# Optimization experiments

Measured on AMD Instinct MI355X. Metric: run time of the kernel, lower is better.

Reference implementation:

```python
import jax, jax.numpy as jnp
import numpy as np

DIM = 512; D_STATE = 8; D_CONV = 3; EXPAND = 1; WIN = 7; N = WIN * WIN
D_INNER = EXPAND * DIM; D_HALF = D_INNER // 2
DT_RANK = -(-DIM // 16)  # 32
E = DT_RANK + 2 * D_STATE  # 48
B_WIN = 512


def _diag_flat(w):
    idx = []
    for s in range(2 * w - 1):
        for r in range(max(0, s - (w - 1)), min(w - 1, s) + 1):
            idx.append(r * w + (s - r))
    return np.array(idx, dtype=np.int32)


def _anti_flat(w):
    idx = []
    for s in range(2 * w - 1):
        for r in range(max(0, s - (w - 1)), min(w - 1, s) + 1):
            c = s - r
            idx.append(r * w + (w - 1 - c))
    return np.array(idx, dtype=np.int32)

DIAG_IDX = jnp.asarray(_diag_flat(WIN))
ANTI_IDX = jnp.asarray(_anti_flat(WIN))
V_IDX = jnp.asarray(np.arange(N).reshape(WIN, WIN).T.reshape(-1).astype(np.int32))


def setup_inputs() -> dict:
    key = jax.random.key(0)
    ks = iter(jax.random.split(key, 32))
    f32 = jnp.float32
    def lin_w(k, out_d, in_d):
        return (jax.random.normal(k, (out_d, in_d), f32) * (in_d ** -0.5)).astype(f32)
    inp = {}
    inp['tokens'] = jax.random.normal(next(ks), (B_WIN, N, DIM), f32)
    for nm in ['pre_h', 'pre_v', 'pre_d', 'pre_a', 'post_h', 'post_v', 'post_d', 'post_a']:
        inp[nm + '_w'] = lin_w(next(ks), DIM, DIM)
        inp[nm + '_b'] = jnp.zeros((DIM,), f32)
    inp['in_proj_w'] = lin_w(next(ks), D_INNER, DIM)
    inp['conv_x_w'] = jax.random.normal(next(ks), (D_HALF, 1, D_CONV), f32) * (D_CONV ** -0.5)
    inp['conv_x_b'] = jnp.zeros((D_HALF,), f32)
    inp['conv_z_w'] = jax.random.normal(next(ks), (D_HALF, 1, D_CONV), f32) * (D_CONV ** -0.5)
    inp['conv_z_b'] = jnp.zeros((D_HALF,), f32)
    inp['x_proj_w'] = lin_w(next(ks), E, D_HALF)
    inp['ln_w'] = jnp.ones((E,), f32)
    inp['ln_b'] = jnp.zeros((E,), f32)
    dt_std = DT_RANK ** -0.5
    inp['dt_proj_w'] = jax.random.uniform(next(ks), (D_HALF, DT_RANK), f32, -dt_std, dt_std)
    u = jax.random.uniform(next(ks), (D_HALF,), f32)
    dt = jnp.clip(jnp.exp(u * (np.log(0.1) - np.log(0.001)) + np.log(0.001)), 1e-4, None)
    inp['dt_proj_b'] = dt + jnp.log(-jnp.expm1(-dt))
    inp['A_log'] = jnp.tile(jnp.log(jnp.arange(1, D_STATE + 1, dtype=f32))[None, :], (D_HALF, 1))
    inp['D_param'] = jnp.ones((D_HALF,), f32)
    inp['out_proj_w'] = lin_w(next(ks), DIM, D_INNER)
    inp['gate_logits'] = jnp.zeros((4,), f32)
    return inp


def _linear(x, W, b=None):
    y = x @ W.T
    return y if b is None else y + b


def _dwconv_same(x, w, b):
    # x: (b, d, l), w: (d, 1, k) depthwise, cross-correlation like torch
    y = jax.lax.conv_general_dilated(x, w, window_strides=(1,), padding='SAME',
                                     dimension_numbers=('NCH', 'OIH', 'NCH'),
                                     feature_group_count=x.shape[1])
    return y + b[None, :, None]


def _layernorm(x, g, b, eps=1e-5):
    m = jnp.mean(x, -1, keepdims=True)
    v = jnp.var(x, -1, keepdims=True)
    return (x - m) * jax.lax.rsqrt(v + eps) * g + b


def _selective_scan(u, delta, A, Bm, Cm, D, delta_bias):
    # u, delta: (b,d,l); A: (d,n); Bm, Cm: (b,n,l); D: (d,)
    delta = jax.nn.softplus(delta + delta_bias[None, :, None])
    u_l = jnp.moveaxis(u, 2, 0)       # (l,b,d)
    d_l = jnp.moveaxis(delta, 2, 0)   # (l,b,d)
    B_l = jnp.moveaxis(Bm, 2, 0)      # (l,b,n)
    C_l = jnp.moveaxis(Cm, 2, 0)      # (l,b,n)
    h0 = jnp.zeros((u.shape[0], u.shape[1], A.shape[1]), u.dtype)  # (b,d,n)

    def step(h, t):
        dt_t, u_t, B_t, C_t = t
        dA = jnp.exp(dt_t[:, :, None] * A[None])          # (b,d,n)
        dBu = dt_t[:, :, None] * B_t[:, None, :] * u_t[:, :, None]
        h = h * dA + dBu
        y = jnp.einsum('bdn,bn->bd', h, C_t)
        return h, y

    _, ys = jax.lax.scan(step, h0, (d_l, u_l, B_l, C_l))
    y = jnp.moveaxis(ys, 0, 2)  # (b,d,l)
    return y + D[None, :, None] * u


def _mamba_core(x_seq, p):
    b, L, _ = x_seq.shape
    xz = _linear(x_seq, p['in_proj_w'])              # (b,l,d_inner)
    xz = jnp.swapaxes(xz, 1, 2)                      # (b,d_inner,l)
    x, z = jnp.split(xz, 2, axis=1)                  # each (b,d_half,l)
    x_conv = jax.nn.silu(_dwconv_same(x, p['conv_x_w'], p['conv_x_b']))
    z_conv = jax.nn.silu(_dwconv_same(z, p['conv_z_w'], p['conv_z_b']))
    A = -jnp.exp(p['A_log'])
    x_dbl = jnp.einsum('bdl,ed->ble', x_conv, p['x_proj_w'])  # (b,l,E)
    x_dbl = _layernorm(x_dbl, p['ln_w'], p['ln_b'])
    dt, Bm, Cm = jnp.split(x_dbl, [DT_RANK, DT_RANK + D_STATE], axis=-1)
    dt = jnp.swapaxes(_linear(dt, p['dt_proj_w']), 1, 2)      # (b,d_half,l)
    Bm = jnp.swapaxes(Bm, 1, 2)                                # (b,n,l)
    Cm = jnp.swapaxes(Cm, 1, 2)
    y = _selective_scan(x_conv, dt, A, Bm, Cm, p['D_param'], p['dt_proj_b'])
    y = jnp.nan_to_num(y)
    y = jnp.concatenate([y, z_conv], axis=1)                   # (b,d_inner,l)
    y = jnp.swapaxes(y, 1, 2)
    return _linear(y, p['out_proj_w'])


def reference(tokens, pre_h_w, pre_h_b, pre_v_w, pre_v_b, pre_d_w, pre_d_b,
              pre_a_w, pre_a_b, in_proj_w, conv_x_w, conv_x_b, conv_z_w, conv_z_b,
              x_proj_w, ln_w, ln_b, dt_proj_w, dt_proj_b, A_log, D_param,
              out_proj_w, post_h_w, post_h_b, post_v_w, post_v_b, post_d_w,
              post_d_b, post_a_w, post_a_b, gate_logits):
    p = dict(in_proj_w=in_proj_w, conv_x_w=conv_x_w, conv_x_b=conv_x_b,
             conv_z_w=conv_z_w, conv_z_b=conv_z_b, x_proj_w=x_proj_w,
             ln_w=ln_w, ln_b=ln_b, dt_proj_w=dt_proj_w, dt_proj_b=dt_proj_b,
             A_log=A_log, D_param=D_param, out_proj_w=out_proj_w)
    rh = _linear(tokens, pre_h_w, pre_h_b)
    rv = _linear(tokens, pre_v_w, pre_v_b)[:, V_IDX, :]
    rd = _linear(tokens, pre_d_w, pre_d_b)[:, DIAG_IDX, :]
    ra = _linear(tokens, pre_a_w, pre_a_b)[:, ANTI_IDX, :]
    r_all = jnp.concatenate([rh, rv, rd, ra], axis=0)
    y_all = _mamba_core(r_all, p)
    yh, yv, yd, ya = jnp.split(y_all, 4, axis=0)
    yh = _linear(yh, post_h_w, post_h_b)
    yv = _linear(yv, post_v_w, post_v_b)
    yd = _linear(yd, post_d_w, post_d_b)
    ya = _linear(ya, post_a_w, post_a_b)
    g = jax.nn.softmax(gate_logits)
    return g[0] * yh + g[1] * yv + g[2] * yd + g[3] * ya
```

## Files before the change

kernel.cpp:

```cpp
#include <hip/hip_runtime.h>
#include <stdint.h>

typedef __attribute__((ext_vector_type(8))) short bf16x8;
typedef __attribute__((ext_vector_type(4))) float f32x4;

__device__ __forceinline__ float bf2f(short u){
  union { float f; uint32_t i; } v; v.i = ((uint32_t)(uint16_t)u) << 16; return v.f;
}
__device__ __forceinline__ short f2bf(float x){
  union { float f; uint32_t i; } v; v.f = x;
  uint32_t r = v.i + 0x7FFFu + ((v.i >> 16) & 1u);
  return (short)(r >> 16);
}

__device__ __forceinline__ void gl_lds16(const short* g, short* l){
  __builtin_amdgcn_global_load_lds(
      (__attribute__((address_space(1))) void*)(short*)g,
      (__attribute__((address_space(3))) void*)l, 16, 0, 0);
}

__device__ const int d_DIAG[49] = {0,1,7,2,8,14,3,9,15,21,4,10,16,22,28,5,11,17,23,29,35,
  6,12,18,24,30,36,42,13,19,25,31,37,43,20,26,32,38,44,27,33,39,45,34,40,46,41,47,48};
__device__ const int d_ANTI[49] = {6,5,13,4,12,20,3,11,19,27,2,10,18,26,34,1,9,17,25,33,41,
  0,8,16,24,32,40,48,7,15,23,31,39,47,14,22,30,38,46,21,29,37,45,28,36,44,35,43,42};

__device__ __forceinline__ int perm_idx(int g, int l){
  if (g == 0) return l;
  if (g == 1) return (l % 7) * 7 + l / 7;
  if (g == 2) return d_DIAG[l];
  return d_ANTI[l];
}

template<int NT>
__device__ __forceinline__ void kloop_pf(
    const short* a0, const short* a1, const short* b0, const short* b1,
    int lds0, int lds1, short* As, short* Bs,
    int quad, int mr, int wm, int wn, f32x4 acc[4][4])
{
  auto STAGE = [&](int t){
    int b = t % 3;
    gl_lds16(a0 + t*32, As + b*4096 + lds0);
    gl_lds16(a1 + t*32, As + b*4096 + lds1);
    gl_lds16(b0 + t*32, Bs + b*4096 + lds0);
    gl_lds16(b1 + t*32, Bs + b*4096 + lds1);
  };
  int sw = (quad ^ ((mr >> 1) & 3)) * 8;
  STAGE(0); STAGE(1);
  for (int t = 0; t < NT; ++t){
    if (t + 2 < NT){
      STAGE(t + 2);
      asm volatile("s_waitcnt vmcnt(8)" ::: "memory");
    } else if (t + 1 < NT){
      asm volatile("s_waitcnt vmcnt(4)" ::: "memory");
    } else {
      asm volatile("s_waitcnt vmcnt(0)" ::: "memory");
    }
    __builtin_amdgcn_s_barrier();
    __builtin_amdgcn_sched_barrier(0);
    const short* Ab = As + (t % 3) * 4096;
    const short* Bb = Bs + (t % 3) * 4096;
    bf16x8 af[4], bfr[4];
    #pragma unroll
    for (int x = 0; x < 4; x++){
      af[x]  = *(const bf16x8*)(Ab + (wm + x*16 + mr)*32 + sw);
      bfr[x] = *(const bf16x8*)(Bb + (wn + x*16 + mr)*32 + sw);
    }
    #pragma unroll
    for (int mt = 0; mt < 4; mt++)
      #pragma unroll
      for (int nt2 = 0; nt2 < 4; nt2++)
        acc[mt][nt2] = __builtin_amdgcn_mfma_f32_16x16x32_bf16(af[mt], bfr[nt2], acc[mt][nt2],0,0,0);
    __builtin_amdgcn_sched_barrier(0);
    __builtin_amdgcn_s_barrier();
  }
}

__global__ __launch_bounds__(256) void k_conv_all(
    const float* __restrict__ in_proj,
    const float* __restrict__ pw0, const float* __restrict__ pw1,
    const float* __restrict__ pw2, const float* __restrict__ pw3,
    const float* __restrict__ xpw, const float* __restrict__ dtw,
    short* __restrict__ inp_bf, short* __restrict__ postw_bf,
    short* __restrict__ xpw_bf, short* __restrict__ dtw_bf)
{
  int q = blockIdx.x*256 + threadIdx.x;
  const float* src; short* dst; int off;
  if (q < 65536){ src = in_proj; dst = inp_bf; off = q; }
  else if (q < 65536 + 262144){
    int r = q - 65536; int g = r >> 16; int loc = r & 65535;
    src = (g==0)?pw0:(g==1)?pw1:(g==2)?pw2:pw3;
    dst = postw_bf + g*262144; off = loc;
  }
  else if (q < 65536 + 262144 + 3072){ src = xpw; dst = xpw_bf; off = q - (65536+262144); }
  else { src = dtw; dst = dtw_bf; off = q - (65536+262144+3072); }
  float4 v = *(const float4*)(src + off*4);
  uint32_t p0 = (uint32_t)(uint16_t)f2bf(v.x) | ((uint32_t)(uint16_t)f2bf(v.y) << 16);
  uint32_t p1 = (uint32_t)(uint16_t)f2bf(v.z) | ((uint32_t)(uint16_t)f2bf(v.w) << 16);
  uint2 p; p.x = p0; p.y = p1;
  *(uint2*)(dst + off*4) = p;
}

__global__ __launch_bounds__(256) void k_transp(
    const float* __restrict__ pw0, const float* __restrict__ pw1,
    const float* __restrict__ pw2, const float* __restrict__ pw3,
    const float* __restrict__ outp,
    short* __restrict__ wpreT, short* __restrict__ woutT)
{
  __shared__ float tile[64][65];
  int which = blockIdx.y;
  const float* src = (which==0)?pw0:(which==1)?pw1:(which==2)?pw2:(which==3)?pw3:outp;
  short* dst = (which < 4) ? (wpreT + which*262144) : woutT;
  int bi = blockIdx.x >> 3, bj = blockIdx.x & 7;
  int r0 = bi*64, c0 = bj*64;
  int t = threadIdx.x;
  int row = t >> 2, cg = t & 3;
  const float4* s4 = (const float4*)(src + (r0+row)*512 + c0 + cg*16);
  #pragma unroll
  for (int i=0;i<4;i++){
    float4 v = s4[i];
    tile[row][cg*16 + i*4 + 0] = v.x;
    tile[row][cg*16 + i*4 + 1] = v.y;
    tile[row][cg*16 + i*4 + 2] = v.z;
    tile[row][cg*16 + i*4 + 3] = v.w;
  }
  __syncthreads();
  int oc = t >> 2;
  short tmp[16];
  #pragma unroll
  for (int i=0;i<16;i++) tmp[i] = f2bf(tile[cg*16 + i][oc]);
  short* dp = dst + (size_t)(c0+oc)*512 + r0 + cg*16;
  *(bf16x8*)(dp)     = *(bf16x8*)tmp;
  *(bf16x8*)(dp + 8) = *((bf16x8*)tmp + 1);
}

__global__ __launch_bounds__(256) void k_tok(const float* __restrict__ t, short* __restrict__ o){
  int i = (blockIdx.x*256 + threadIdx.x) * 4;
  float4 v = *(const float4*)(t + i);
  uint32_t p0 = (uint32_t)(uint16_t)f2bf(v.x) | ((uint32_t)(uint16_t)f2bf(v.y) << 16);
  uint32_t p1 = (uint32_t)(uint16_t)f2bf(v.z) | ((uint32_t)(uint16_t)f2bf(v.w) << 16);
  uint2 p; p.x = p0; p.y = p1;
  *(uint2*)(o + i) = p;
}

__global__ __launch_bounds__(256) void k_bxz_gains(const float* __restrict__ in_proj,
    const float* __restrict__ b0, const float* __restrict__ b1,
    const float* __restrict__ b2, const float* __restrict__ b3,
    const float* __restrict__ gl,
    const float* __restrict__ pb0, const float* __restrict__ pb1,
    const float* __restrict__ pb2, const float* __restrict__ pb3,
    float* __restrict__ bxz, float* __restrict__ gains, float* __restrict__ biasc)
{
  if (blockIdx.x < 8){
    int idx = blockIdx.x*256 + threadIdx.x;
    int g = idx >> 9, i = idx & 511;
    const float* bb = (g==0)?b0:(g==1)?b1:(g==2)?b2:b3;
    float s = 0.f;
    for (int t=0;t<512;t++) s += in_proj[i*512+t]*bb[t];
    bxz[idx] = s;
  } else {
    float m = fmaxf(fmaxf(gl[0], gl[1]), fmaxf(gl[2], gl[3]));
    float e0 = expf(gl[0]-m), e1 = expf(gl[1]-m), e2 = expf(gl[2]-m), e3 = expf(gl[3]-m);
    float s = e0+e1+e2+e3;
    float g0 = e0/s, g1 = e1/s, g2 = e2/s, g3 = e3/s;
    int t = threadIdx.x;
    if (t == 0){ gains[0]=g0; gains[1]=g1; gains[2]=g2; gains[3]=g3; }
    biasc[t]     = g0*pb0[t]     + g1*pb1[t]     + g2*pb2[t]     + g3*pb3[t];
    biasc[t+256] = g0*pb0[t+256] + g1*pb1[t+256] + g2*pb2[t+256] + g3*pb3[t+256];
  }
}

__device__ __forceinline__ void mfma_2x4_k(const short* a0, const short* a1,
    const short* b0, const short* b1, const short* b2, const short* b3,
    int K, f32x4 acc[2][4])
{
  for (int k0 = 0; k0 < K; k0 += 32){
    bf16x8 av0 = *(const bf16x8*)(a0 + k0);
    bf16x8 av1 = *(const bf16x8*)(a1 + k0);
    bf16x8 bv0 = *(const bf16x8*)(b0 + k0);
    bf16x8 bv1 = *(const bf16x8*)(b1 + k0);
    bf16x8 bv2 = *(const bf16x8*)(b2 + k0);
    bf16x8 bv3 = *(const bf16x8*)(b3 + k0);
    acc[0][0] = __builtin_amdgcn_mfma_f32_16x16x32_bf16(av0, bv0, acc[0][0],0,0,0);
    acc[0][1] = __builtin_amdgcn_mfma_f32_16x16x32_bf16(av0, bv1, acc[0][1],0,0,0);
    acc[0][2] = __builtin_amdgcn_mfma_f32_16x16x32_bf16(av0, bv2, acc[0][2],0,0,0);
    acc[0][3] = __builtin_amdgcn_mfma_f32_16x16x32_bf16(av0, bv3, acc[0][3],0,0,0);
    acc[1][0] = __builtin_amdgcn_mfma_f32_16x16x32_bf16(av1, bv0, acc[1][0],0,0,0);
    acc[1][1] = __builtin_amdgcn_mfma_f32_16x16x32_bf16(av1, bv1, acc[1][1],0,0,0);
    acc[1][2] = __builtin_amdgcn_mfma_f32_16x16x32_bf16(av1, bv2, acc[1][2],0,0,0);
    acc[1][3] = __builtin_amdgcn_mfma_f32_16x16x32_bf16(av1, bv3, acc[1][3],0,0,0);
  }
}

__global__ __launch_bounds__(256) void k_wfuse(const short* __restrict__ inp_bf,
    const short* __restrict__ wpreT, const short* __restrict__ postw_bf,
    const short* __restrict__ woutT, const float* __restrict__ gains,
    short* __restrict__ wxz, short* __restrict__ wogc)
{
  int z = blockIdx.z; int g = z & 3, which = z >> 2;
  int bn = blockIdx.x * 64, bm = blockIdx.y * 128;
  int lane = threadIdx.x & 63, wave = threadIdx.x >> 6;
  int mr = lane & 15, qk = (lane >> 4) * 8, quad = lane >> 4;
  const short* Am = which ? (postw_bf + g*262144) : inp_bf;
  const short* Bm = which ? woutT : (wpreT + g*262144);
  const short* a0 = Am + (bm + wave*32 + mr)*512 + qk;
  const short* a1 = a0 + 16*512;
  const short* b0 = Bm + (bn +  0 + mr)*512 + qk;
  const short* b1 = Bm + (bn + 16 + mr)*512 + qk;
  const short* b2 = Bm + (bn + 32 + mr)*512 + qk;
  const short* b3 = Bm + (bn + 48 + mr)*512 + qk;
  f32x4 acc[2][4] = {};
  mfma_2x4_k(a0, a1, b0, b1, b2, b3, 512, acc);
  float gain = which ? gains[g] : 1.f;
  #pragma unroll
  for (int s=0;s<2;s++)
    #pragma unroll
    for (int t=0;t<4;t++)
      #pragma unroll
      for (int r=0;r<4;r++){
        int row = bm + wave*32 + s*16 + quad*4 + r;
        int col = bn + t*16 + mr;
        if (which) wogc[row*2048 + g*512 + col] = f2bf(gain * acc[s][t][r]);
        else       wxz[g*262144 + row*512 + col] = f2bf(acc[s][t][r]);
      }
}

__global__ __launch_bounds__(256) void k_gemm1(const short* __restrict__ tok,
    const short* __restrict__ wxz, const float* __restrict__ bxz, short* __restrict__ xz)
{
  __shared__ __align__(16) short As[12288];
  __shared__ __align__(16) short Bs[12288];
  int g = blockIdx.z;
  int bid = blockIdx.x;
  int swz = (bid & 7) * 98 + (bid >> 3);
  int bn = (swz & 3) * 128, bm = (swz >> 2) * 128;
  int tid = threadIdx.x, lane = tid & 63, wave = tid >> 6;

  const short* aG[2]; const short* bG[2]; int ldsOff[2];
  #pragma unroll
  for (int i = 0; i < 2; i++){
    int c = wave*2 + i;
    int r = c*16 + (lane >> 2);
    int ch = ((lane & 3) ^ ((lane >> 3) & 3)) * 8;
    int grow = bm + r;
    int b = grow / 49, l = grow - b*49;
    int sl = perm_idx(g, l);
    aG[i] = tok + ((size_t)(b*49 + sl))*512 + ch;
    bG[i] = wxz + (size_t)g*262144 + (size_t)(bn + r)*512 + ch;
    ldsOff[i] = c*512;
  }

  int mr = lane & 15, quad = lane >> 4;
  int wm = (wave & 1)*64, wn = (wave >> 1)*64;
  f32x4 acc[4][4] = {};

  kloop_pf<16>(aG[0], aG[1], bG[0], bG[1], ldsOff[0], ldsOff[1],
               As, Bs, quad, mr, wm, wn, acc);

  #pragma unroll
  for (int mt = 0; mt < 4; mt++)
    #pragma unroll
    for (int rr = 0; rr < 4; rr++){
      int row = bm + wm + mt*16 + quad*4 + rr;
      int b = row / 49, l = row - b*49;
      size_t orow = ((size_t)(g*512 + b)*49 + l)*512;
      #pragma unroll
      for (int nt = 0; nt < 4; nt++){
        int col = bn + wn + nt*16 + mr;
        xz[orow + col] = f2bf(acc[mt][nt][rr] + bxz[g*512 + col]);
      }
    }
}

__global__ __launch_bounds__(256) void k_conv(const short* __restrict__ xz,
    const float* __restrict__ cxw, const float* __restrict__ cxb,
    const float* __restrict__ czw, const float* __restrict__ czb,
    short* __restrict__ ycat)
{
  int t = threadIdx.x;
  int oct = t & 63, lstart = t >> 6;
  int ch0 = oct * 8;
  bool isx = ch0 < 256;
  int cc0 = isx ? ch0 : ch0 - 256;
  const float* wsrc = isx ? cxw : czw;
  const float* bsrc = isx ? cxb : czb;
  float w0[8], w1[8], w2[8], bb[8];
  #pragma unroll
  for (int e=0;e<8;e++){
    w0[e] = wsrc[(cc0+e)*3]; w1[e] = wsrc[(cc0+e)*3+1]; w2[e] = wsrc[(cc0+e)*3+2];
    bb[e] = bsrc[cc0+e];
  }
  int gb = blockIdx.x; int g = gb >> 9, b = gb & 511;
  const short* src = xz + (size_t)gb*25088 + ch0;
  short* dst = ycat + (size_t)(b*49)*2048 + g*512 + ch0;
  for (int l = lstart; l < 49; l += 4){
    bf16x8 vm = {}, vp = {};
    bf16x8 v0 = *(const bf16x8*)(src + l*512);
    if (l > 0)  vm = *(const bf16x8*)(src + (l-1)*512);
    if (l < 48) vp = *(const bf16x8*)(src + (l+1)*512);
    short ov[8];
    #pragma unroll
    for (int e=0;e<8;e++){
      float x = w0[e]*bf2f(vm[e]) + w1[e]*bf2f(v0[e]) + w2[e]*bf2f(vp[e]) + bb[e];
      ov[e] = f2bf(x / (1.f + __expf(-x)));
    }
    *(bf16x8*)(dst + l*2048) = *(bf16x8*)ov;
  }
}

__global__ __launch_bounds__(256) void k_xproj(const short* __restrict__ ycat,
    const short* __restrict__ xpw_bf, const float* __restrict__ lnw, const float* __restrict__ lnb,
    const short* __restrict__ dtw_bf, const float* __restrict__ dtb,
    short* __restrict__ dtln, float* __restrict__ bc)
{
  __shared__ __align__(16) char smem[36864];
  float* xd = (float*)smem;
  short* xln = (short*)(smem + 26624);

  int bm = blockIdx.x * 128;
  int g = bm / 25088;
  int tid = threadIdx.x, lane = tid & 63, w = tid >> 6;
  int mr = lane & 15, quad = lane >> 4, qk = quad * 8;

  {
    const short* ap[2];
    #pragma unroll
    for (int s=0;s<2;s++)
      ap[s] = ycat + (size_t)(bm - g*25088 + w*32 + s*16 + mr)*2048 + g*512 + qk;
    f32x4 acc[2][3] = {};
    #pragma unroll
    for (int k0 = 0; k0 < 256; k0 += 32){
      bf16x8 av[2];
      #pragma unroll
      for (int s=0;s<2;s++) av[s] = *(const bf16x8*)(ap[s] + k0);
      #pragma unroll
      for (int t=0;t<3;t++){
        bf16x8 bv = *(const bf16x8*)(xpw_bf + (t*16 + mr)*256 + qk + k0);
        #pragma unroll
        for (int s=0;s<2;s++)
          acc[s][t] = __builtin_amdgcn_mfma_f32_16x16x32_bf16(av[s], bv, acc[s][t],0,0,0);
      }
    }
    #pragma unroll
    for (int s=0;s<2;s++)
      #pragma unroll
      for (int t=0;t<3;t++)
        #pragma unroll
        for (int r=0;r<4;r++)
          xd[(w*32 + s*16 + quad*4 + r)*52 + t*16 + mr] = acc[s][t][r];
  }
  __syncthreads();

  if (tid < 128){
    f32x4* xr4 = (f32x4*)(xd + tid*52);
    f32x4 s = xr4[0];
    #pragma unroll
    for (int i=1;i<12;i++) s += xr4[i];
    float m = (s[0]+s[1]+s[2]+s[3]) * (1.f/48.f);
    f32x4 vs = {};
    #pragma unroll
    for (int i=0;i<12;i++){ f32x4 d = xr4[i] - m; vs += d*d; }
    float var = (vs[0]+vs[1]+vs[2]+vs[3]) * (1.f/48.f);
    float rstd = rsqrtf(var + 1e-5f);
    const f32x4* g4 = (const f32x4*)lnw;
    const f32x4* b4 = (const f32x4*)lnb;
    uint32_t* xlr = (uint32_t*)(xln + tid*40);
    #pragma unroll
    for (int i=0;i<8;i++){
      f32x4 v = (xr4[i] - m) * rstd * g4[i] + b4[i];
      xlr[2*i]   = (uint32_t)(uint16_t)f2bf(v[0]) | ((uint32_t)(uint16_t)f2bf(v[1]) << 16);
      xlr[2*i+1] = (uint32_t)(uint16_t)f2bf(v[2]) | ((uint32_t)(uint16_t)f2bf(v[3]) << 16);
    }
    f32x4* bco = (f32x4*)(bc + (size_t)(bm + tid)*16);
    #pragma unroll
    for (int i=8;i<12;i++)
      bco[i-8] = (xr4[i] - m) * rstd * g4[i] + b4[i];
  }
  __syncthreads();

  {
    bf16x8 a[2];
    #pragma unroll
    for (int s=0;s<2;s++)
      a[s] = *(const bf16x8*)(xln + (w*32 + s*16 + mr)*40 + qk);
    #pragma unroll 4
    for (int nt=0; nt<16; nt++){
      int col = nt*16 + mr;
      bf16x8 bv = *(const bf16x8*)(dtw_bf + col*32 + qk);
      float dtbv = dtb[col];
      #pragma unroll
      for (int s=0;s<2;s++){
        f32x4 acc = {};
        acc = __builtin_amdgcn_mfma_f32_16x16x32_bf16(a[s], bv, acc,0,0,0);
        #pragma unroll
        for (int r=0;r<4;r++){
          int grow = bm + w*32 + s*16 + quad*4 + r;
          float dtv = acc[r] + dtbv;
          float e  = __expf(dtv);
          float sp = __logf(1.f + e);
          float delta = (dtv > 15.f) ? dtv : sp;
          dtln[(size_t)grow*256 + col] = f2bf(delta);
        }
      }
    }
  }
}

__global__ __launch_bounds__(256) void k_scan(short* __restrict__ ycat,
    const short* __restrict__ dtln, const float* __restrict__ bc,
    const float* __restrict__ Alog, const float* __restrict__ Dp)
{
  __shared__ __align__(16) float bcs[784];
  int gb = blockIdx.x; int g = gb >> 9, b = gb & 511;
  int d = threadIdx.x;
  if (d < 196) ((f32x4*)bcs)[d] = ((const f32x4*)(bc + (size_t)gb*784))[d];
  __syncthreads();

  float A[8], h[8];
  {
    f32x4 a0 = *(const f32x4*)(Alog + d*8);
    f32x4 a1 = *(const f32x4*)(Alog + d*8 + 4);
    #pragma unroll
    for (int n=0;n<4;n++){ A[n] = -__expf(a0[n]); A[n+4] = -__expf(a1[n]); h[n]=0.f; h[n+4]=0.f; }
  }
  float Dpar = Dp[d];

  const short* dptr = dtln + (size_t)gb*49*256 + d;
  short* uptr = ycat + (size_t)(b*49)*2048 + g*512 + d;

  float dn = bf2f(dptr[0]);
  float un = bf2f(uptr[0]);
  for (int l=0;l<49;l++){
    float delta = dn, u = un;
    if (l < 48){ dn = bf2f(dptr[(l+1)*256]); un = bf2f(uptr[(l+1)*2048]); }
    const f32x4* bcr = (const f32x4*)(bcs + l*16);
    f32x4 B0 = bcr[0], B1 = bcr[1], C0 = bcr[2], C1 = bcr[3];
    float du = delta * u;
    float y = 0.f;
    #pragma unroll
    for (int n=0;n<4;n++){
      h[n] = h[n]*__expf(delta*A[n]) + du*B0[n];
      y += h[n]*C0[n];
    }
    #pragma unroll
    for (int n=0;n<4;n++){
      h[n+4] = h[n+4]*__expf(delta*A[n+4]) + du*B1[n];
      y += h[n+4]*C1[n];
    }
    uptr[l*2048] = f2bf(y + Dpar*u);
  }
}

__global__ __launch_bounds__(256) void k_gemmF(const short* __restrict__ ycat,
    const short* __restrict__ wogc, const float* __restrict__ biasc,
    float* __restrict__ out)
{
  __shared__ __align__(16) short As[12288];
  __shared__ __align__(16) short Bs[12288];
  int bid = blockIdx.x;
  int swz = (bid & 7) * 98 + (bid >> 3);
  int bn = (swz & 3) * 128, bm = (swz >> 2) * 128;
  int tid = threadIdx.x, lane = tid & 63, wave = tid >> 6;

  const short* aG[2]; const short* bG[2]; int ldsOff[2];
  #pragma unroll
  for (int i = 0; i < 2; i++){
    int c = wave*2 + i;
    int r = c*16 + (lane >> 2);
    int ch = ((lane & 3) ^ ((lane >> 3) & 3)) * 8;
    aG[i] = ycat + (size_t)(bm + r)*2048 + ch;
    bG[i] = wogc + (size_t)(bn + r)*2048 + ch;
    ldsOff[i] = c*512;
  }

  int mr = lane & 15, quad = lane >> 4;
  int wm = (wave & 1)*64, wn = (wave >> 1)*64;
  f32x4 acc[4][4] = {};

  kloop_pf<64>(aG[0], aG[1], bG[0], bG[1], ldsOff[0], ldsOff[1],
               As, Bs, quad, mr, wm, wn, acc);

  #pragma unroll
  for (int mt = 0; mt < 4; mt++)
    #pragma unroll
    for (int rr = 0; rr < 4; rr++){
      int row = bm + wm + mt*16 + quad*4 + rr;
      float* orow = out + (size_t)row*512;
      #pragma unroll
      for (int nt = 0; nt < 4; nt++){
        int col = bn + wn + nt*16 + mr;
        orow[col] = acc[mt][nt][rr] + biasc[col];
      }
    }
}

extern "C" void kernel_launch(void* const* d_in, const int* in_sizes, int n_in,
                              void* d_out, int out_size, void* d_ws, size_t ws_size,
                              hipStream_t stream)
{
  const float* tokens    = (const float*)d_in[0];
  const float* pre_w[4]  = {(const float*)d_in[1], (const float*)d_in[3], (const float*)d_in[5], (const float*)d_in[7]};
  const float* pre_b[4]  = {(const float*)d_in[2], (const float*)d_in[4], (const float*)d_in[6], (const float*)d_in[8]};
  const float* post_w[4] = {(const float*)d_in[9], (const float*)d_in[11], (const float*)d_in[13], (const float*)d_in[15]};
  const float* post_b[4] = {(const float*)d_in[10], (const float*)d_in[12], (const float*)d_in[14], (const float*)d_in[16]};
  const float* in_proj   = (const float*)d_in[17];
  const float* conv_x_w  = (const float*)d_in[18];
  const float* conv_x_b  = (const float*)d_in[19];
  const float* conv_z_w  = (const float*)d_in[20];
  const float* conv_z_b  = (const float*)d_in[21];
  const float* x_proj_w  = (const float*)d_in[22];
  const float* ln_w      = (const float*)d_in[23];
  const float* ln_b      = (const float*)d_in[24];
  const float* dt_proj_w = (const float*)d_in[25];
  const float* dt_proj_b = (const float*)d_in[26];
  const float* A_log     = (const float*)d_in[27];
  const float* D_param   = (const float*)d_in[28];
  const float* out_proj  = (const float*)d_in[29];
  const float* gate_log  = (const float*)d_in[30];

  char* ws = (char*)d_ws;
  size_t o = 0;
  short* tok_bf   = (short*)(ws + o); o += 25690112;
  short* wpreT    = (short*)(ws + o); o += 2097152;
  short* inp_bf   = (short*)(ws + o); o += 524288;
  short* postw_bf = (short*)(ws + o); o += 2097152;
  short* woutT    = (short*)(ws + o); o += 524288;
  short* wogc     = (short*)(ws + o); o += 2097152;
  short* wxz      = (short*)(ws + o); o += 2097152;
  short* xpw_bf   = (short*)(ws + o); o += 24576;
  short* dtw_bf   = (short*)(ws + o); o += 16384;
  float* bxz      = (float*)(ws + o); o += 8192;
  float* gains    = (float*)(ws + o); o += 64;
  float* biasc    = (float*)(ws + o); o += 2048;
  size_t xz_off = o;
  short* xz       = (short*)(ws + o); o += 102760448;
  short* ycat     = (short*)(ws + o); o += 102760448;
  short* dtln     = (short*)(ws + xz_off);
  float* bc       = (float*)(ws + xz_off + 51380224);

  k_conv_all<<<1300, 256, 0, stream>>>(in_proj,
      post_w[0], post_w[1], post_w[2], post_w[3],
      x_proj_w, dt_proj_w, inp_bf, postw_bf, xpw_bf, dtw_bf);
  k_transp<<<dim3(64,5), 256, 0, stream>>>(pre_w[0], pre_w[1], pre_w[2], pre_w[3],
      out_proj, wpreT, woutT);
  k_tok<<<12544, 256, 0, stream>>>(tokens, tok_bf);
  k_bxz_gains<<<9, 256, 0, stream>>>(in_proj, pre_b[0], pre_b[1], pre_b[2], pre_b[3],
      gate_log, post_b[0], post_b[1], post_b[2], post_b[3], bxz, gains, biasc);
  k_wfuse<<<dim3(8,4,8), 256, 0, stream>>>(inp_bf, wpreT, postw_bf, woutT, gains, wxz, wogc);
  k_gemm1<<<dim3(784,1,4), 256, 0, stream>>>(tok_bf, wxz, bxz, xz);
  k_conv<<<2048, 256, 0, stream>>>(xz, conv_x_w, conv_x_b, conv_z_w, conv_z_b, ycat);
  k_xproj<<<784, 256, 0, stream>>>(ycat, xpw_bf, ln_w, ln_b, dtw_bf, dt_proj_b, dtln, bc);
  k_scan<<<2048, 256, 0, stream>>>(ycat, dtln, bc, A_log, D_param);
  k_gemmF<<<dim3(784), 256, 0, stream>>>(ycat, wogc, biasc, (float*)d_out);
}
```

Baseline: 527.0 us.

## Shrink GEMM tiles to 64x128 with double-buffered unified LDS staging

Both the input-projection GEMM and the final output GEMM now use 64x128 block tiles instead of 128x128, doubling the grid size. The LDS pipeline drops from triple-buffered separate A/B arrays to a single double-buffered array, and each thread issues three async loads per stage. The aim is more blocks per CU and lower LDS and register use for better occupancy and latency hiding. In exchange, each block does less MFMA work per load, so global traffic for the weight operand rises and only one stage of prefetch is in flight.

Result: no change. 526.2 us (-0.2%).

```diff
diff --git a/kernel.cpp b/kernel.cpp
--- a/kernel.cpp
+++ b/kernel.cpp
@@ -32,41 +32,38 @@
 }
 
 template<int NT>
-__device__ __forceinline__ void kloop_pf(
-    const short* a0, const short* a1, const short* b0, const short* b1,
-    int lds0, int lds1, short* As, short* Bs,
-    int quad, int mr, int wm, int wn, f32x4 acc[4][4])
+__device__ __forceinline__ void kloop64(
+    const short* g0, const short* g1, const short* g2,
+    int l0, int l1, int l2, short* S,
+    int quad, int mr, int wm, int wn, f32x4 acc[2][4])
 {
   auto STAGE = [&](int t){
-    int b = t % 3;
-    gl_lds16(a0 + t*32, As + b*4096 + lds0);
-    gl_lds16(a1 + t*32, As + b*4096 + lds1);
-    gl_lds16(b0 + t*32, Bs + b*4096 + lds0);
-    gl_lds16(b1 + t*32, Bs + b*4096 + lds1);
+    int b = (t & 1) * 6144;
+    gl_lds16(g0 + t*32, S + b + l0);
+    gl_lds16(g1 + t*32, S + b + l1);
+    gl_lds16(g2 + t*32, S + b + l2);
   };
   int sw = (quad ^ ((mr >> 1) & 3)) * 8;
-  STAGE(0); STAGE(1);
+  STAGE(0);
   for (int t = 0; t < NT; ++t){
-    if (t + 2 < NT){
-      STAGE(t + 2);
-      asm volatile("s_waitcnt vmcnt(8)" ::: "memory");
-    } else if (t + 1 < NT){
-      asm volatile("s_waitcnt vmcnt(4)" ::: "memory");
+    if (t + 1 < NT){
+      STAGE(t + 1);
+      asm volatile("s_waitcnt vmcnt(3)" ::: "memory");
     } else {
       asm volatile("s_waitcnt vmcnt(0)" ::: "memory");
     }
     __builtin_amdgcn_s_barrier();
     __builtin_amdgcn_sched_barrier(0);
-    const short* Ab = As + (t % 3) * 4096;
-    const short* Bb = Bs + (t % 3) * 4096;
-    bf16x8 af[4], bfr[4];
-    #pragma unroll
-    for (int x = 0; x < 4; x++){
-      af[x]  = *(const bf16x8*)(Ab + (wm + x*16 + mr)*32 + sw);
-      bfr[x] = *(const bf16x8*)(Bb + (wn + x*16 + mr)*32 + sw);
-    }
-    #pragma unroll
-    for (int mt = 0; mt < 4; mt++)
+    const short* Sb = S + (t & 1) * 6144;
+    bf16x8 af[2], bfr[4];
+    #pragma unroll
+    for (int x = 0; x < 2; x++)
+      af[x]  = *(const bf16x8*)(Sb + (wm + x*16 + mr)*32 + sw);
+    #pragma unroll
+    for (int x = 0; x < 4; x++)
+      bfr[x] = *(const bf16x8*)(Sb + 2048 + (wn + x*16 + mr)*32 + sw);
+    #pragma unroll
+    for (int mt = 0; mt < 2; mt++)
       #pragma unroll
       for (int nt2 = 0; nt2 < 4; nt2++)
         acc[mt][nt2] = __builtin_amdgcn_mfma_f32_16x16x32_bf16(af[mt], bfr[nt2], acc[mt][nt2],0,0,0);
@@ -227,37 +224,41 @@
 __global__ __launch_bounds__(256) void k_gemm1(const short* __restrict__ tok,
     const short* __restrict__ wxz, const float* __restrict__ bxz, short* __restrict__ xz)
 {
-  __shared__ __align__(16) short As[12288];
-  __shared__ __align__(16) short Bs[12288];
+  __shared__ __align__(16) short S[12288];
   int g = blockIdx.z;
   int bid = blockIdx.x;
-  int swz = (bid & 7) * 98 + (bid >> 3);
-  int bn = (swz & 3) * 128, bm = (swz >> 2) * 128;
+  int swz = (bid & 7) * 196 + (bid >> 3);
+  int bn = (swz & 3) * 128, bm = (swz >> 2) * 64;
   int tid = threadIdx.x, lane = tid & 63, wave = tid >> 6;
 
-  const short* aG[2]; const short* bG[2]; int ldsOff[2];
+  const short* gp[3]; int lo[3];
+  {
+    int rr16 = lane >> 2;
+    int ch = ((lane & 3) ^ ((lane >> 3) & 3)) * 8;
+    #pragma unroll
+    for (int i = 0; i < 3; i++){
+      int c = wave*3 + i;
+      if (c < 4){
+        int grow = bm + c*16 + rr16;
+        int b = grow / 49, l = grow - b*49;
+        int sl = perm_idx(g, l);
+        gp[i] = tok + ((size_t)(b*49 + sl))*512 + ch;
+        lo[i] = c*512;
+      } else {
+        gp[i] = wxz + (size_t)g*262144 + (size_t)(bn + (c-4)*16 + rr16)*512 + ch;
+        lo[i] = 2048 + (c-4)*512;
+      }
+    }
+  }
+
+  int mr = lane & 15, quad = lane >> 4;
+  int wm = (wave & 1)*32, wn = (wave >> 1)*64;
+  f32x4 acc[2][4] = {};
+
+  kloop64<16>(gp[0], gp[1], gp[2], lo[0], lo[1], lo[2], S, quad, mr, wm, wn, acc);
+
   #pragma unroll
-  for (int i = 0; i < 2; i++){
-    int c = wave*2 + i;
-    int r = c*16 + (lane >> 2);
-    int ch = ((lane & 3) ^ ((lane >> 3) & 3)) * 8;
-    int grow = bm + r;
-    int b = grow / 49, l = grow - b*49;
-    int sl = perm_idx(g, l);
-    aG[i] = tok + ((size_t)(b*49 + sl))*512 + ch;
-    bG[i] = wxz + (size_t)g*262144 + (size_t)(bn + r)*512 + ch;
-    ldsOff[i] = c*512;
-  }
-
-  int mr = lane & 15, quad = lane >> 4;
-  int wm = (wave & 1)*64, wn = (wave >> 1)*64;
-  f32x4 acc[4][4] = {};
-
-  kloop_pf<16>(aG[0], aG[1], bG[0], bG[1], ldsOff[0], ldsOff[1],
-               As, Bs, quad, mr, wm, wn, acc);
-
-  #pragma unroll
-  for (int mt = 0; mt < 4; mt++)
+  for (int mt = 0; mt < 2; mt++)
     #pragma unroll
     for (int rr = 0; rr < 4; rr++){
       int row = bm + wm + mt*16 + quad*4 + rr;
@@ -454,33 +455,37 @@
     const short* __restrict__ wogc, const float* __restrict__ biasc,
     float* __restrict__ out)
 {
-  __shared__ __align__(16) short As[12288];
-  __shared__ __align__(16) short Bs[12288];
+  __shared__ __align__(16) short S[12288];
   int bid = blockIdx.x;
-  int swz = (bid & 7) * 98 + (bid >> 3);
-  int bn = (swz & 3) * 128, bm = (swz >> 2) * 128;
+  int swz = (bid & 7) * 196 + (bid >> 3);
+  int bn = (swz & 3) * 128, bm = (swz >> 2) * 64;
   int tid = threadIdx.x, lane = tid & 63, wave = tid >> 6;
 
-  const short* aG[2]; const short* bG[2]; int ldsOff[2];
+  const short* gp[3]; int lo[3];
+  {
+    int rr16 = lane >> 2;
+    int ch = ((lane & 3) ^ ((lane >> 3) & 3)) * 8;
+    #pragma unroll
+    for (int i = 0; i < 3; i++){
+      int c = wave*3 + i;
+      if (c < 4){
+        gp[i] = ycat + (size_t)(bm + c*16 + rr16)*2048 + ch;
+        lo[i] = c*512;
+      } else {
+        gp[i] = wogc + (size_t)(bn + (c-4)*16 + rr16)*2048 + ch;
+        lo[i] = 2048 + (c-4)*512;
+      }
+    }
+  }
+
+  int mr = lane & 15, quad = lane >> 4;
+  int wm = (wave & 1)*32, wn = (wave >> 1)*64;
+  f32x4 acc[2][4] = {};
+
+  kloop64<64>(gp[0], gp[1], gp[2], lo[0], lo[1], lo[2], S, quad, mr, wm, wn, acc);
+
   #pragma unroll
-  for (int i = 0; i < 2; i++){
-    int c = wave*2 + i;
-    int r = c*16 + (lane >> 2);
-    int ch = ((lane & 3) ^ ((lane >> 3) & 3)) * 8;
-    aG[i] = ycat + (size_t)(bm + r)*2048 + ch;
-    bG[i] = wogc + (size_t)(bn + r)*2048 + ch;
-    ldsOff[i] = c*512;
-  }
-
-  int mr = lane & 15, quad = lane >> 4;
-  int wm = (wave & 1)*64, wn = (wave >> 1)*64;
-  f32x4 acc[4][4] = {};
-
-  kloop_pf<64>(aG[0], aG[1], bG[0], bG[1], ldsOff[0], ldsOff[1],
-               As, Bs, quad, mr, wm, wn, acc);
-
-  #pragma unroll
-  for (int mt = 0; mt < 4; mt++)
+  for (int mt = 0; mt < 2; mt++)
     #pragma unroll
     for (int rr = 0; rr < 4; rr++){
       int row = bm + wm + mt*16 + quad*4 + rr;
@@ -546,9 +551,9 @@
   k_bxz_gains<<<9, 256, 0, stream>>>(in_proj, pre_b[0], pre_b[1], pre_b[2], pre_b[3],
       gate_log, post_b[0], post_b[1], post_b[2], post_b[3], bxz, gains, biasc);
   k_wfuse<<<dim3(8,4,8), 256, 0, stream>>>(inp_bf, wpreT, postw_bf, woutT, gains, wxz, wogc);
-  k_gemm1<<<dim3(784,1,4), 256, 0, stream>>>(tok_bf, wxz, bxz, xz);
+  k_gemm1<<<dim3(1568,1,4), 256, 0, stream>>>(tok_bf, wxz, bxz, xz);
   k_conv<<<2048, 256, 0, stream>>>(xz, conv_x_w, conv_x_b, conv_z_w, conv_z_b, ycat);
   k_xproj<<<784, 256, 0, stream>>>(ycat, xpw_bf, ln_w, ln_b, dtw_bf, dt_proj_b, dtln, bc);
   k_scan<<<2048, 256, 0, stream>>>(ycat, dtln, bc, A_log, D_param);
-  k_gemmF<<<dim3(784), 256, 0, stream>>>(ycat, wogc, biasc, (float*)d_out);
-}
+  k_gemmF<<<dim3(1568), 256, 0, stream>>>(ycat, wogc, biasc, (float*)d_out);
+}
```

## Enlarge GEMM tiles to 256x256 with 8 waves and double-buffered staged loads

Applied to the files above, without the earlier changes.

Both large GEMMs move from 128x128 tiles with 4 waves and triple buffering to 256x256 tiles with 8 waves, double-buffered LDS, and global-to-LDS loads for the next k-step spread across the compute phases. The goal is more operand reuse per tile and less global/L2 traffic per MFMA. The cost is more accumulator registers and lower occupancy. The final GEMM also drops to 196 blocks, fewer than the CU count, which can leave compute units idle.

Result: faster. 513.1 us (-2.6%).

```diff
diff --git a/kernel.cpp b/kernel.cpp
--- a/kernel.cpp
+++ b/kernel.cpp
@@ -32,45 +32,51 @@
 }
 
 template<int NT>
-__device__ __forceinline__ void kloop_pf(
-    const short* a0, const short* a1, const short* b0, const short* b1,
-    int lds0, int lds1, short* As, short* Bs,
-    int quad, int mr, int wm, int wn, f32x4 acc[4][4])
-{
-  auto STAGE = [&](int t){
-    int b = t % 3;
-    gl_lds16(a0 + t*32, As + b*4096 + lds0);
-    gl_lds16(a1 + t*32, As + b*4096 + lds1);
-    gl_lds16(b0 + t*32, Bs + b*4096 + lds0);
-    gl_lds16(b1 + t*32, Bs + b*4096 + lds1);
+__device__ __forceinline__ void kcore256(
+    const short* aU0, const short* aU1, const short* bU0, const short* bU1,
+    short* S, int w, int lane, f32x4 acc[8][4])
+{
+  int wr = w >> 2, wc = w & 3;
+  int mr = lane & 15, quad = lane >> 4;
+  int sw = (quad ^ ((mr >> 1) & 3)) * 8;
+  auto STAGE = [&](int u, int t){
+    short* base = S + (t & 1) * 16384;
+    if      (u == 0) gl_lds16(aU0 + t*32, base + (w*32)*32);
+    else if (u == 1) gl_lds16(aU1 + t*32, base + (w*32 + 16)*32);
+    else if (u == 2) gl_lds16(bU0 + t*32, base + 8192 + (w*32)*32);
+    else             gl_lds16(bU1 + t*32, base + 8192 + (w*32 + 16)*32);
   };
-  int sw = (quad ^ ((mr >> 1) & 3)) * 8;
-  STAGE(0); STAGE(1);
+  STAGE(0,0); STAGE(1,0); STAGE(2,0); STAGE(3,0);
+  if (NT > 1){ STAGE(0,1); STAGE(1,1); }
+  asm volatile("s_waitcnt vmcnt(2)" ::: "memory");
+  __builtin_amdgcn_s_barrier();
   for (int t = 0; t < NT; ++t){
-    if (t + 2 < NT){
-      STAGE(t + 2);
-      asm volatile("s_waitcnt vmcnt(8)" ::: "memory");
-    } else if (t + 1 < NT){
-      asm volatile("s_waitcnt vmcnt(4)" ::: "memory");
-    } else {
+    const short* Ab = S + (t & 1) * 16384;
+    const short* Bb = Ab + 8192;
+    bf16x8 bfr[4];
+    #pragma unroll
+    for (int nf = 0; nf < 4; ++nf)
+      bfr[nf] = *(const bf16x8*)(Bb + (wc*64 + nf*16 + mr)*32 + sw);
+    #pragma unroll
+    for (int ph = 0; ph < 4; ++ph){
+      bf16x8 af[2];
+      #pragma unroll
+      for (int mi = 0; mi < 2; ++mi)
+        af[mi] = *(const bf16x8*)(Ab + (wr*128 + (ph*2+mi)*16 + mr)*32 + sw);
+      if (ph < 2 && t+1 < NT) STAGE(2+ph, t+1);
+      #pragma unroll
+      for (int mi = 0; mi < 2; ++mi)
+        #pragma unroll
+        for (int nf = 0; nf < 4; ++nf)
+          acc[ph*2+mi][nf] = __builtin_amdgcn_mfma_f32_16x16x32_bf16(af[mi], bfr[nf], acc[ph*2+mi][nf],0,0,0);
+    }
+    __builtin_amdgcn_s_barrier();
+    if (t+2 < NT){
+      STAGE(0, t+2); STAGE(1, t+2);
+      asm volatile("s_waitcnt vmcnt(2)" ::: "memory");
+    } else if (t+1 < NT){
       asm volatile("s_waitcnt vmcnt(0)" ::: "memory");
     }
-    __builtin_amdgcn_s_barrier();
-    __builtin_amdgcn_sched_barrier(0);
-    const short* Ab = As + (t % 3) * 4096;
-    const short* Bb = Bs + (t % 3) * 4096;
-    bf16x8 af[4], bfr[4];
-    #pragma unroll
-    for (int x = 0; x < 4; x++){
-      af[x]  = *(const bf16x8*)(Ab + (wm + x*16 + mr)*32 + sw);
-      bfr[x] = *(const bf16x8*)(Bb + (wn + x*16 + mr)*32 + sw);
-    }
-    #pragma unroll
-    for (int mt = 0; mt < 4; mt++)
-      #pragma unroll
-      for (int nt2 = 0; nt2 < 4; nt2++)
-        acc[mt][nt2] = __builtin_amdgcn_mfma_f32_16x16x32_bf16(af[mt], bfr[nt2], acc[mt][nt2],0,0,0);
-    __builtin_amdgcn_sched_barrier(0);
     __builtin_amdgcn_s_barrier();
   }
 }
@@ -224,49 +230,44 @@
       }
 }
 
-__global__ __launch_bounds__(256) void k_gemm1(const short* __restrict__ tok,
+__global__ __launch_bounds__(512) void k_gemm1(const short* __restrict__ tok,
     const short* __restrict__ wxz, const float* __restrict__ bxz, short* __restrict__ xz)
 {
-  __shared__ __align__(16) short As[12288];
-  __shared__ __align__(16) short Bs[12288];
-  int g = blockIdx.z;
+  __shared__ __align__(16) short S[32768];
   int bid = blockIdx.x;
   int swz = (bid & 7) * 98 + (bid >> 3);
-  int bn = (swz & 3) * 128, bm = (swz >> 2) * 128;
-  int tid = threadIdx.x, lane = tid & 63, wave = tid >> 6;
-
-  const short* aG[2]; const short* bG[2]; int ldsOff[2];
-  #pragma unroll
-  for (int i = 0; i < 2; i++){
-    int c = wave*2 + i;
-    int r = c*16 + (lane >> 2);
-    int ch = ((lane & 3) ^ ((lane >> 3) & 3)) * 8;
-    int grow = bm + r;
-    int b = grow / 49, l = grow - b*49;
-    int sl = perm_idx(g, l);
-    aG[i] = tok + ((size_t)(b*49 + sl))*512 + ch;
-    bG[i] = wxz + (size_t)g*262144 + (size_t)(bn + r)*512 + ch;
-    ldsOff[i] = c*512;
-  }
-
-  int mr = lane & 15, quad = lane >> 4;
-  int wm = (wave & 1)*64, wn = (wave >> 1)*64;
-  f32x4 acc[4][4] = {};
-
-  kloop_pf<16>(aG[0], aG[1], bG[0], bG[1], ldsOff[0], ldsOff[1],
-               As, Bs, quad, mr, wm, wn, acc);
-
-  #pragma unroll
-  for (int mt = 0; mt < 4; mt++)
-    #pragma unroll
-    for (int rr = 0; rr < 4; rr++){
-      int row = bm + wm + mt*16 + quad*4 + rr;
+  int g = swz / 196, rem = swz - g*196;
+  int bm = (rem >> 1) * 256, bn = (rem & 1) * 256;
+  int tid = threadIdx.x, lane = tid & 63, w = tid >> 6;
+
+  int rl = lane >> 2;
+  int gch = ((lane & 3) ^ ((lane >> 3) & 3)) * 8;
+  const short* aU[2];
+  #pragma unroll
+  for (int j = 0; j < 2; ++j){
+    int grow = bm + w*32 + j*16 + rl;
+    int b = grow / 49, l49 = grow - b*49;
+    int sl = perm_idx(g, l49);
+    aU[j] = tok + ((size_t)(b*49 + sl))*512 + gch;
+  }
+  const short* bU0 = wxz + (size_t)g*262144 + (size_t)(bn + w*32      + rl)*512 + gch;
+  const short* bU1 = wxz + (size_t)g*262144 + (size_t)(bn + w*32 + 16 + rl)*512 + gch;
+
+  f32x4 acc[8][4] = {};
+  kcore256<16>(aU[0], aU[1], bU0, bU1, S, w, lane, acc);
+
+  int wr = w >> 2, wc = w & 3, mr = lane & 15, quad = lane >> 4;
+  #pragma unroll
+  for (int mf = 0; mf < 8; ++mf)
+    #pragma unroll
+    for (int rr = 0; rr < 4; ++rr){
+      int row = bm + wr*128 + mf*16 + quad*4 + rr;
       int b = row / 49, l = row - b*49;
       size_t orow = ((size_t)(g*512 + b)*49 + l)*512;
       #pragma unroll
-      for (int nt = 0; nt < 4; nt++){
-        int col = bn + wn + nt*16 + mr;
-        xz[orow + col] = f2bf(acc[mt][nt][rr] + bxz[g*512 + col]);
+      for (int nf = 0; nf < 4; ++nf){
+        int col = bn + wc*64 + nf*16 + mr;
+        xz[orow + col] = f2bf(acc[mf][nf][rr] + bxz[g*512 + col]);
       }
     }
 }
@@ -450,45 +451,36 @@
   }
 }
 
-__global__ __launch_bounds__(256) void k_gemmF(const short* __restrict__ ycat,
+__global__ __launch_bounds__(512) void k_gemmF(const short* __restrict__ ycat,
     const short* __restrict__ wogc, const float* __restrict__ biasc,
     float* __restrict__ out)
 {
-  __shared__ __align__(16) short As[12288];
-  __shared__ __align__(16) short Bs[12288];
+  __shared__ __align__(16) short S[32768];
   int bid = blockIdx.x;
-  int swz = (bid & 7) * 98 + (bid >> 3);
-  int bn = (swz & 3) * 128, bm = (swz >> 2) * 128;
-  int tid = threadIdx.x, lane = tid & 63, wave = tid >> 6;
-
-  const short* aG[2]; const short* bG[2]; int ldsOff[2];
-  #pragma unroll
-  for (int i = 0; i < 2; i++){
-    int c = wave*2 + i;
-    int r = c*16 + (lane >> 2);
-    int ch = ((lane & 3) ^ ((lane >> 3) & 3)) * 8;
-    aG[i] = ycat + (size_t)(bm + r)*2048 + ch;
-    bG[i] = wogc + (size_t)(bn + r)*2048 + ch;
-    ldsOff[i] = c*512;
-  }
-
-  int mr = lane & 15, quad = lane >> 4;
-  int wm = (wave & 1)*64, wn = (wave >> 1)*64;
-  f32x4 acc[4][4] = {};
-
-  kloop_pf<64>(aG[0], aG[1], bG[0], bG[1], ldsOff[0], ldsOff[1],
-               As, Bs, quad, mr, wm, wn, acc);
-
-  #pragma unroll
-  for (int mt = 0; mt < 4; mt++)
-    #pragma unroll
-    for (int rr = 0; rr < 4; rr++){
-      int row = bm + wm + mt*16 + quad*4 + rr;
+  int bm = (bid >> 1) * 256, bn = (bid & 1) * 256;
+  int tid = threadIdx.x, lane = tid & 63, w = tid >> 6;
+
+  int rl = lane >> 2;
+  int gch = ((lane & 3) ^ ((lane >> 3) & 3)) * 8;
+  const short* aU0 = ycat + (size_t)(bm + w*32      + rl)*2048 + gch;
+  const short* aU1 = ycat + (size_t)(bm + w*32 + 16 + rl)*2048 + gch;
+  const short* bU0 = wogc + (size_t)(bn + w*32      + rl)*2048 + gch;
+  const short* bU1 = wogc + (size_t)(bn + w*32 + 16 + rl)*2048 + gch;
+
+  f32x4 acc[8][4] = {};
+  kcore256<64>(aU0, aU1, bU0, bU1, S, w, lane, acc);
+
+  int wr = w >> 2, wc = w & 3, mr = lane & 15, quad = lane >> 4;
+  #pragma unroll
+  for (int mf = 0; mf < 8; ++mf)
+    #pragma unroll
+    for (int rr = 0; rr < 4; ++rr){
+      int row = bm + wr*128 + mf*16 + quad*4 + rr;
       float* orow = out + (size_t)row*512;
       #pragma unroll
-      for (int nt = 0; nt < 4; nt++){
-        int col = bn + wn + nt*16 + mr;
-        orow[col] = acc[mt][nt][rr] + biasc[col];
+      for (int nf = 0; nf < 4; ++nf){
+        int col = bn + wc*64 + nf*16 + mr;
+        orow[col] = acc[mf][nf][rr] + biasc[col];
       }
     }
 }
@@ -546,9 +538,9 @@
   k_bxz_gains<<<9, 256, 0, stream>>>(in_proj, pre_b[0], pre_b[1], pre_b[2], pre_b[3],
       gate_log, post_b[0], post_b[1], post_b[2], post_b[3], bxz, gains, biasc);
   k_wfuse<<<dim3(8,4,8), 256, 0, stream>>>(inp_bf, wpreT, postw_bf, woutT, gains, wxz, wogc);
-  k_gemm1<<<dim3(784,1,4), 256, 0, stream>>>(tok_bf, wxz, bxz, xz);
+  k_gemm1<<<dim3(784), 512, 0, stream>>>(tok_bf, wxz, bxz, xz);
   k_conv<<<2048, 256, 0, stream>>>(xz, conv_x_w, conv_x_b, conv_z_w, conv_z_b, ycat);
   k_xproj<<<784, 256, 0, stream>>>(ycat, xpw_bf, ln_w, ln_b, dtw_bf, dt_proj_b, dtln, bc);
   k_scan<<<2048, 256, 0, stream>>>(ycat, dtln, bc, A_log, D_param);
-  k_gemmF<<<dim3(784), 256, 0, stream>>>(ycat, wogc, biasc, (float*)d_out);
-}
+  k_gemmF<<<dim3(196), 512, 0, stream>>>(ycat, wogc, biasc, (float*)d_out);
+}
```
